# Kernel optimization log

Measured on AMD Instinct MI355X. Metric: run time of the kernel, lower is better.

The kernel has to match this reference:

```python
import jax, jax.numpy as jnp
import numpy as np

B, S, D = 2, 2048, 2048
NH = 16
HD = D // NH  # 128
MAX_POS = 4096
ROPE_THETA = 10000.0


def rotate_half(x):
    x1, x2 = x[..., : x.shape[-1] // 2], x[..., x.shape[-1] // 2 :]
    return jnp.concatenate((-x2, x1), axis=-1)


def rope_tables(dtype=jnp.float32):
    inv_freq = 1.0 / (ROPE_THETA ** (jnp.arange(0, HD, 2, dtype=jnp.float32) / HD))
    t = jnp.arange(MAX_POS, dtype=jnp.float32)
    freqs = jnp.outer(t, inv_freq)              # [MAX_POS, HD/2]
    emb = jnp.concatenate((freqs, freqs), axis=-1)  # [MAX_POS, HD]
    return jnp.cos(emb).astype(dtype), jnp.sin(emb).astype(dtype)


def setup_inputs() -> dict:
    key = jax.random.key(0)
    ks = jax.random.split(key, 9)
    sc = 0.02
    return {
        "hidden_states": jax.random.normal(ks[0], (B, S, D), jnp.float32),
        "position_ids": jnp.arange(B * S, dtype=jnp.int32).reshape(B, S),
        "Wq": jax.random.normal(ks[1], (D, D), jnp.float32) * sc,
        "bq": jax.random.normal(ks[2], (D,), jnp.float32) * sc,
        "Wk": jax.random.normal(ks[3], (D, D), jnp.float32) * sc,
        "bk": jax.random.normal(ks[4], (D,), jnp.float32) * sc,
        "Wv": jax.random.normal(ks[5], (D, D), jnp.float32) * sc,
        "bv": jax.random.normal(ks[6], (D,), jnp.float32) * sc,
        "Wo": jax.random.normal(ks[7], (D, D), jnp.float32) * sc,
    }


def reference(hidden_states, position_ids, Wq, bq, Wk, bk, Wv, bv, Wo):
    b, s, _ = hidden_states.shape
    # projections (torch Linear: x @ W.T + b)
    q = (hidden_states @ Wq.T + bq).reshape(b, s, NH, HD).transpose(0, 2, 1, 3)
    k = (hidden_states @ Wk.T + bk).reshape(b, s, NH, HD).transpose(0, 2, 1, 3)
    v = (hidden_states @ Wv.T + bv).reshape(b, s, NH, HD).transpose(0, 2, 1, 3)
    # RoPE
    cos_t, sin_t = rope_tables(hidden_states.dtype)
    cos = cos_t[position_ids][:, None, :, :]  # [B,1,S,HD]
    sin = sin_t[position_ids][:, None, :, :]
    q = q * cos + rotate_half(q) * sin
    k = k * cos + rotate_half(k) * sin
    # NOTE: faithful to the source bug — softmax is computed but its result is
    # discarded; the AV matmul uses the UNNORMALIZED scaled scores.
    attn_weights = jnp.einsum("bhqd,bhkd->bhqk", q, k) / (HD ** 0.5)
    _ = jax.nn.softmax(attn_weights.astype(jnp.float32), axis=-1)  # dead, as in source
    attn_output = jnp.einsum("bhqk,bhkd->bhqd", attn_weights, v)
    attn_output = attn_output.transpose(0, 2, 1, 3).reshape(b, s, D)
    return attn_output @ Wo.T
```

## Files before the change

kernel.cpp:

```cpp
#include <hip/hip_runtime.h>
#include <hip/hip_bf16.h>


typedef __attribute__((ext_vector_type(8))) short bf16x8s;
typedef __attribute__((ext_vector_type(4))) float f32x4;

__device__ __forceinline__ ushort f2bf(float f) {
    union { float f; unsigned int u; } x; x.f = f;
    unsigned int u = x.u;
    unsigned int r = (u + 0x7fffu + ((u >> 16) & 1u)) >> 16;
    return (ushort)r;
}
__device__ __forceinline__ float b2f(ushort u) {
    union { unsigned int u; float f; } x; x.u = ((unsigned int)u) << 16;
    return x.f;
}

__device__ __forceinline__ void gload_lds16(const void* g, void* l) {
    __builtin_amdgcn_global_load_lds((__attribute__((address_space(1))) const void*)g,
                                     (__attribute__((address_space(3))) void*)l, 16, 0, 0);
}

template<bool BIAS, bool OBF16>
__global__ __launch_bounds__(512, 2)
void gemm256(const ushort* __restrict__ A, const ushort* __restrict__ B,
             const float* __restrict__ bias, void* __restrict__ Cv,
             int K, int lda, int ldb, int ldc,
             long sAb, long sBb, long sCb)
{
    __shared__ char smem[131072];

    int z = blockIdx.z;
    const ushort* Ab = A + (size_t)sAb * z;
    const ushort* Bb = B + (size_t)sBb * z;
    size_t Coff = (size_t)sCb * z;

    int nwgx = gridDim.x;
    int nwg = nwgx * gridDim.y;
    int wg = blockIdx.y * nwgx + blockIdx.x;
    int swz = ((nwg & 7) == 0) ? (wg & 7) * (nwg >> 3) + (wg >> 3) : wg;
    int m0 = (swz % nwgx) * 256;
    int n0 = (swz / nwgx) * 256;

    int tid = threadIdx.x;
    int l = tid & 63, wid = tid >> 6;
    int wm = (wid >> 2) * 128;
    int wn = (wid & 3) * 64;
    int lr = l & 15, lj = l >> 4;

    int offA[8], offB[4];
#pragma unroll
    for (int m = 0; m < 8; m++) {
        int r = wm + m * 16 + lr;
        offA[m] = (r >> 1) * 128 + (((((r & 1) << 2) | lj) ^ ((r >> 1) & 7)) << 4);
    }
#pragma unroll
    for (int n = 0; n < 4; n++) {
        int r = wn + n * 16 + lr;
        offB[n] = (r >> 1) * 128 + (((((r & 1) << 2) | lj) ^ ((r >> 1) & 7)) << 4);
    }

    unsigned srcA0, srcA1, srcB0, srcB1;
    int dst0 = tid * 16, dst1 = dst0 + 8192;
    {
        int c0 = tid, c1 = tid + 512;
        int pr0 = c0 >> 3, up0 = (c0 & 7) ^ (pr0 & 7);
        int r0 = (pr0 << 1) | (up0 >> 2), j0 = up0 & 3;
        int pr1 = c1 >> 3, up1 = (c1 & 7) ^ (pr1 & 7);
        int r1 = (pr1 << 1) | (up1 >> 2), j1 = up1 & 3;
        srcA0 = (unsigned)(m0 + r0) * lda + j0 * 8;
        srcA1 = (unsigned)(m0 + r1) * lda + j1 * 8;
        srcB0 = (unsigned)(n0 + r0) * ldb + j0 * 8;
        srcB1 = (unsigned)(n0 + r1) * ldb + j1 * 8;
    }

    f32x4 acc[8][4];
#pragma unroll
    for (int m = 0; m < 8; m++)
#pragma unroll
        for (int n = 0; n < 4; n++)
            acc[m][n] = (f32x4){0.f, 0.f, 0.f, 0.f};

    int NT = K >> 6;

#define STAGE_A(ldsbyte, eoff) { \
    gload_lds16(Ab + srcA0 + (eoff), smem + (ldsbyte) + dst0); \
    gload_lds16(Ab + srcA1 + (eoff), smem + (ldsbyte) + dst1); }
#define STAGE_B(ldsbyte, eoff) { \
    gload_lds16(Bb + srcB0 + (eoff), smem + (ldsbyte) + dst0); \
    gload_lds16(Bb + srcB1 + (eoff), smem + (ldsbyte) + dst1); }
#define MFMA_HALF(mb) { \
    __builtin_amdgcn_s_setprio(1); \
    _Pragma("unroll") \
    for (int m = 0; m < 4; m++) \
        _Pragma("unroll") \
        for (int n = 0; n < 4; n++) \
            acc[(mb) + m][n] = __builtin_amdgcn_mfma_f32_16x16x32_bf16( \
                af[(mb) + m], bf[n], acc[(mb) + m][n], 0, 0, 0); \
    __builtin_amdgcn_s_setprio(0); }

    STAGE_A(0, 0);
    STAGE_B(32768, 0);
    STAGE_A(16384, 32);
    STAGE_B(49152, 32);
    asm volatile("s_waitcnt vmcnt(4)" ::: "memory");
    __builtin_amdgcn_s_barrier();

    for (int t = 0; t < NT; ++t) {
        int lb = (t & 1) << 16;
        int pb = lb ^ 65536;
        bool pf = (t + 1 < NT);
        unsigned eo = (unsigned)(t + 1) * 64;
        bf16x8s af[8], bf[4];

#pragma unroll
        for (int m = 0; m < 4; m++)
            af[m] = *(const bf16x8s*)(smem + lb + offA[m]);
#pragma unroll
        for (int n = 0; n < 4; n++)
            bf[n] = *(const bf16x8s*)(smem + lb + 32768 + offB[n]);
        if (pf) STAGE_A(pb, eo);
#pragma unroll
        for (int m = 4; m < 8; m++)
            af[m] = *(const bf16x8s*)(smem + lb + offA[m]);
        asm volatile("s_waitcnt lgkmcnt(4)" ::: "memory");
        __builtin_amdgcn_sched_barrier(0);
        MFMA_HALF(0);
        asm volatile("s_waitcnt lgkmcnt(0)" ::: "memory");
        __builtin_amdgcn_sched_barrier(0);
        MFMA_HALF(4);
        if (pf) STAGE_B(pb + 32768, eo);
        if (pf) asm volatile("s_waitcnt vmcnt(4)" ::: "memory");
        else    asm volatile("s_waitcnt vmcnt(0)" ::: "memory");
        __builtin_amdgcn_s_barrier();

#pragma unroll
        for (int m = 0; m < 4; m++)
            af[m] = *(const bf16x8s*)(smem + lb + 16384 + offA[m]);
#pragma unroll
        for (int n = 0; n < 4; n++)
            bf[n] = *(const bf16x8s*)(smem + lb + 49152 + offB[n]);
        if (pf) STAGE_A(pb + 16384, eo + 32);
#pragma unroll
        for (int m = 4; m < 8; m++)
            af[m] = *(const bf16x8s*)(smem + lb + 16384 + offA[m]);
        asm volatile("s_waitcnt lgkmcnt(4)" ::: "memory");
        __builtin_amdgcn_sched_barrier(0);
        MFMA_HALF(0);
        asm volatile("s_waitcnt lgkmcnt(0)" ::: "memory");
        __builtin_amdgcn_sched_barrier(0);
        MFMA_HALF(4);
        if (pf) {
            STAGE_B(pb + 49152, eo + 32);
            asm volatile("s_waitcnt vmcnt(4)" ::: "memory");
            __builtin_amdgcn_s_barrier();
        }
    }
#undef STAGE_A
#undef STAGE_B
#undef MFMA_HALF

    int rr = lj * 4;
#pragma unroll
    for (int m = 0; m < 8; m++) {
#pragma unroll
        for (int n = 0; n < 4; n++) {
            int gr = m0 + wm + m * 16 + rr;
            int gc = n0 + wn + n * 16 + lr;
            float bv = BIAS ? bias[gc] : 0.f;
#pragma unroll
            for (int r = 0; r < 4; r++) {
                float v = acc[m][n][r] + bv;
                size_t off = Coff + (size_t)(gr + r) * ldc + gc;
                if (OBF16) ((ushort*)Cv)[off] = f2bf(v);
                else       ((float*)Cv)[off]  = v;
            }
        }
    }
}

template<bool BIAS, bool OBF16, int BN>
__global__ __launch_bounds__(256)
void gemm_nt(const ushort* __restrict__ A, const ushort* __restrict__ B,
             const float* __restrict__ bias, void* __restrict__ Cv,
             int K, int lda, int ldb, int ldc, int ZH,
             long sAb, long sAh, long sBb, long sBh, long sCb, long sCh)
{
    __shared__ ushort As[128 * 32];
    __shared__ ushort Bs[BN * 32];

    int z  = blockIdx.z;
    int zb = z / ZH, zh = z - zb * ZH;
    const ushort* Ab = A + (size_t)(sAb * zb + sAh * zh);
    const ushort* Bb = B + (size_t)(sBb * zb + sBh * zh);
    size_t Coff = (size_t)(sCb * zb + sCh * zh);

    int m0 = blockIdx.x * 128, n0 = blockIdx.y * BN;
    int t = threadIdx.x;
    int l = t & 63, w = t >> 6;
    int wm, wn;
    if (BN == 128) { wm = (w >> 1) * 64; wn = (w & 1) * 64; }
    else           { wm = w * 32;        wn = 0; }
    constexpr int FM = (BN == 128) ? 4 : 2;
    constexpr int FN = 4;
    int lr = l & 15, lk = (l >> 4) * 8;

    f32x4 acc[FM][FN];
#pragma unroll
    for (int i = 0; i < FM; i++)
#pragma unroll
        for (int j = 0; j < FN; j++)
            acc[i][j] = (f32x4){0.f, 0.f, 0.f, 0.f};

    int c0 = t, c1 = t + 256;
    int r0 = c0 >> 2, k0c = (c0 & 3) * 8;
    int r1 = c1 >> 2, k1c = (c1 & 3) * 8;

    for (int kt = 0; kt < K; kt += 32) {
        __syncthreads();
        gload_lds16(Ab + (size_t)(m0 + r0) * lda + kt + k0c, &As[c0 * 8]);
        gload_lds16(Ab + (size_t)(m0 + r1) * lda + kt + k1c, &As[c1 * 8]);
        gload_lds16(Bb + (size_t)(n0 + r0) * ldb + kt + k0c, &Bs[c0 * 8]);
        if (BN == 128)
            gload_lds16(Bb + (size_t)(n0 + r1) * ldb + kt + k1c, &Bs[c1 * 8]);
        __syncthreads();

        bf16x8s af[FM], bf[FN];
#pragma unroll
        for (int i = 0; i < FM; i++)
            af[i] = *(const bf16x8s*)&As[(wm + i * 16 + lr) * 32 + lk];
#pragma unroll
        for (int i = 0; i < FN; i++)
            bf[i] = *(const bf16x8s*)&Bs[(wn + i * 16 + lr) * 32 + lk];
#pragma unroll
        for (int mi = 0; mi < FM; mi++)
#pragma unroll
            for (int ni = 0; ni < FN; ni++)
                acc[mi][ni] = __builtin_amdgcn_mfma_f32_16x16x32_bf16(
                    af[mi], bf[ni], acc[mi][ni], 0, 0, 0);
    }

    int rr = (l >> 4) * 4;
#pragma unroll
    for (int mi = 0; mi < FM; mi++) {
#pragma unroll
        for (int ni = 0; ni < FN; ni++) {
            int gr = m0 + wm + mi * 16 + rr;
            int gc = n0 + wn + ni * 16 + lr;
            float bv = BIAS ? bias[gc] : 0.f;
#pragma unroll
            for (int r = 0; r < 4; r++) {
                float v = acc[mi][ni][r] + bv;
                size_t off = Coff + (size_t)(gr + r) * ldc + gc;
                if (OBF16) ((ushort*)Cv)[off] = f2bf(v);
                else       ((float*)Cv)[off]  = v;
            }
        }
    }
}

__global__ __launch_bounds__(256)
void rope_qk(ushort* __restrict__ QKV, const int* __restrict__ pos,
             ushort* __restrict__ QB)
{
    int tid = blockIdx.x * 256 + threadIdx.x;
    int row = tid >> 7;
    int r = tid & 127;
    int h = r >> 3, j = r & 7;
    int d0 = j * 8;
    float p = (float)pos[row];
    size_t qb = (size_t)row * 6144 + h * 128 + d0;

    bf16x8s q1 = *(const bf16x8s*)&QKV[qb];
    bf16x8s q2 = *(const bf16x8s*)&QKV[qb + 64];
    bf16x8s k1 = *(const bf16x8s*)&QKV[qb + 2048];
    bf16x8s k2 = *(const bf16x8s*)&QKV[qb + 2048 + 64];
    bf16x8s oq1, oq2, ok1, ok2;
#pragma unroll
    for (int i = 0; i < 8; i++) {
        float d = (float)(d0 + i);
        float ang = p * exp2f(d * (-13.287712379549449f / 64.0f));
        float s, c;
        sincosf(ang, &s, &c);
        float a = b2f((ushort)q1[i]), b = b2f((ushort)q2[i]);
        oq1[i] = (short)f2bf(a * c - b * s);
        oq2[i] = (short)f2bf(b * c + a * s);
        float e = b2f((ushort)k1[i]), f = b2f((ushort)k2[i]);
        ok1[i] = (short)f2bf(e * c - f * s);
        ok2[i] = (short)f2bf(f * c + e * s);
    }
    size_t ob = (size_t)row * 2048 + h * 128 + d0;
    *(bf16x8s*)&QB[ob]      = oq1;
    *(bf16x8s*)&QB[ob + 64] = oq2;
    *(bf16x8s*)&QKV[qb + 2048]      = ok1;
    *(bf16x8s*)&QKV[qb + 2048 + 64] = ok2;
}

__global__ __launch_bounds__(256)
void ktv_partial(const ushort* __restrict__ QKV, float* __restrict__ part)
{
    int bh = blockIdx.x;
    int b = bh >> 4, h = bh & 15;
    int s0 = blockIdx.y * 128;
    const ushort* Kp = QKV + (size_t)(b * 2048 + s0) * 6144 + 2048 + h * 128;
    const ushort* Vp = Kp + 2048;

    __shared__ ushort Ks[32][128];
    __shared__ ushort Vs[32][128];

    int t = threadIdx.x;
    int tx = t & 15, ty = t >> 4;
    float acc[8][8];
#pragma unroll
    for (int i = 0; i < 8; i++)
#pragma unroll
        for (int j = 0; j < 8; j++) acc[i][j] = 0.f;

    for (int sb = 0; sb < 128; sb += 32) {
        __syncthreads();
#pragma unroll
        for (int i = 0; i < 2; i++) {
            int idx = t + i * 256;
            int rw = idx >> 4, c8 = (idx & 15) * 8;
            *(bf16x8s*)&Ks[rw][c8] = *(const bf16x8s*)&Kp[(size_t)(sb + rw) * 6144 + c8];
            *(bf16x8s*)&Vs[rw][c8] = *(const bf16x8s*)&Vp[(size_t)(sb + rw) * 6144 + c8];
        }
        __syncthreads();
        for (int ss = 0; ss < 32; ss++) {
            bf16x8s kvv = *(const bf16x8s*)&Ks[ss][tx * 8];
            bf16x8s vvv = *(const bf16x8s*)&Vs[ss][ty * 8];
            float kv[8], vv[8];
#pragma unroll
            for (int i = 0; i < 8; i++) { kv[i] = b2f((ushort)kvv[i]); vv[i] = b2f((ushort)vvv[i]); }
#pragma unroll
            for (int i = 0; i < 8; i++)
#pragma unroll
                for (int j = 0; j < 8; j++)
                    acc[i][j] += kv[i] * vv[j];
        }
    }
    float* pp = part + ((size_t)blockIdx.y * 32 + bh) * 16384;
#pragma unroll
    for (int i = 0; i < 8; i++)
#pragma unroll
        for (int j = 0; j < 8; j++)
            pp[(tx * 8 + i) * 128 + (ty * 8 + j)] = acc[i][j];
}

__global__ __launch_bounds__(256)
void reduce_ktv(const float* __restrict__ part, ushort* __restrict__ Mb)
{
    int i = blockIdx.x * 256 + threadIdx.x;
    float s = 0.f;
#pragma unroll
    for (int p = 0; p < 16; p++) s += part[(size_t)p * 524288 + i];
    Mb[i] = f2bf(s * 0.08838834764831845f);
}

__global__ __launch_bounds__(256)
void conv_f32_bf16(const float* __restrict__ in, ushort* __restrict__ out, int n4)
{
    int i = blockIdx.x * 256 + threadIdx.x;
    if (i >= n4) return;
    float4 v = ((const float4*)in)[i];
    ushort4 o;
    o.x = f2bf(v.x); o.y = f2bf(v.y); o.z = f2bf(v.z); o.w = f2bf(v.w);
    ((ushort4*)out)[i] = o;
}

__global__ __launch_bounds__(256)
void conv_weights(const float* __restrict__ w0, const float* __restrict__ w1,
                  const float* __restrict__ w2, const float* __restrict__ w3,
                  ushort* __restrict__ qkv, ushort* __restrict__ wo)
{
    int i = blockIdx.x * 256 + threadIdx.x;
    int id = i >> 20;
    int off = i & 1048575;
    const float* src = (id == 0) ? w0 : (id == 1) ? w1 : (id == 2) ? w2 : w3;
    float4 v = ((const float4*)src)[off];
    ushort4 o;
    o.x = f2bf(v.x); o.y = f2bf(v.y); o.z = f2bf(v.z); o.w = f2bf(v.w);
    if (id < 3) ((ushort4*)qkv)[(size_t)id * 1048576 + off] = o;
    else        ((ushort4*)wo)[off] = o;
}

__global__ __launch_bounds__(256)
void pack_bias(const float* __restrict__ bq, const float* __restrict__ bk,
               const float* __restrict__ bv, float* __restrict__ bqkv)
{
    int i = blockIdx.x * 256 + threadIdx.x;
    float v = (i < 2048) ? bq[i] : (i < 4096) ? bk[i - 2048] : bv[i - 4096];
    bqkv[i] = v;
}

extern "C" void kernel_launch(void* const* d_in, const int* in_sizes, int n_in,
                              void* d_out, int out_size, void* d_ws, size_t ws_size,
                              hipStream_t stream)
{
    const float* hs = (const float*)d_in[0];
    const int*  pos = (const int*)d_in[1];
    const float* Wq = (const float*)d_in[2];
    const float* bq = (const float*)d_in[3];
    const float* Wk = (const float*)d_in[4];
    const float* bk = (const float*)d_in[5];
    const float* Wv = (const float*)d_in[6];
    const float* bv = (const float*)d_in[7];
    const float* Wo = (const float*)d_in[8];
    float* out = (float*)d_out;
    char* ws = (char*)d_ws;

    ushort* HSB  = (ushort*)(ws + 0);
    ushort* QB   = (ushort*)(ws + 0);
    ushort* WQKV = (ushort*)(ws + 16777216);
    ushort* NT   = (ushort*)(ws + 16777216);
    ushort* WOB  = (ushort*)(ws + 41943040);
    float*  BQKV = (float*)(ws + 50331648);
    ushort* QKVB = (ushort*)(ws + 50356224);
    ushort* MB   = (ushort*)(ws + 100687872);
    float*  PART = out;

    dim3 blk(256);

    conv_f32_bf16<<<8192, blk, 0, stream>>>(hs, HSB, 2097152);
    conv_weights<<<16384, blk, 0, stream>>>(Wq, Wk, Wv, Wo, WQKV, WOB);
    pack_bias<<<24, blk, 0, stream>>>(bq, bk, bv, BQKV);

    gemm256<true, true><<<dim3(16, 24, 1), dim3(512), 0, stream>>>(
        HSB, WQKV, BQKV, QKVB, 2048, 2048, 2048, 6144, 0, 0, 0);

    rope_qk<<<2048, blk, 0, stream>>>(QKVB, pos, QB);

    ktv_partial<<<dim3(32, 16, 1), blk, 0, stream>>>(QKVB, PART);
    reduce_ktv<<<2048, blk, 0, stream>>>(PART, MB);

    gemm_nt<false, true, 128><<<dim3(16, 1, 32), blk, 0, stream>>>(
        WOB, MB, nullptr, NT, 128, 2048, 128, 2048, 16,
        0, 128, 262144, 16384, 4194304, 128);

    gemm256<false, false><<<dim3(8, 8, 2), dim3(512), 0, stream>>>(
        QB, NT, nullptr, out, 2048, 2048, 2048, 2048,
        4194304, 4194304, 4194304);
}
```

Before: 382.1 us.

## Shrink gemm256 K-stage to 32, precompute RoPE table, use gemm_nt for output GEMM

The main GEMM drops from a 64-wide K step in two half-stages to a single 32-wide double-buffered stage using 64KB of LDS. Its launch bound rises to 4 blocks per CU, aiming for higher occupancy. RoPE cos/sin values now come from a precomputed table built by a new kernel instead of per-element sincos/exp2. The final output GEMM switches from gemm256 to the 128-tile gemm_nt kernel. The single-stage loop waits on vmcnt(0) every iteration, which weakens load/compute overlap, and the 4-block bound may cause register spills with a 128-float accumulator per thread.

New measurement: 1.473 ms. 3.85x slower.

```diff
diff --git a/kernel.cpp b/kernel.cpp
--- a/kernel.cpp
+++ b/kernel.cpp
@@ -22,13 +22,13 @@
 }
 
 template<bool BIAS, bool OBF16>
-__global__ __launch_bounds__(512, 2)
+__global__ __launch_bounds__(512, 4)
 void gemm256(const ushort* __restrict__ A, const ushort* __restrict__ B,
              const float* __restrict__ bias, void* __restrict__ Cv,
              int K, int lda, int ldb, int ldc,
              long sAb, long sBb, long sCb)
 {
-    __shared__ char smem[131072];
+    __shared__ char smem[65536];
 
     int z = blockIdx.z;
     const ushort* Ab = A + (size_t)sAb * z;
@@ -81,7 +81,7 @@
         for (int n = 0; n < 4; n++)
             acc[m][n] = (f32x4){0.f, 0.f, 0.f, 0.f};
 
-    int NT = K >> 6;
+    int NT = K >> 5;
 
 #define STAGE_A(ldsbyte, eoff) { \
     gload_lds16(Ab + srcA0 + (eoff), smem + (ldsbyte) + dst0); \
@@ -100,61 +100,36 @@
     __builtin_amdgcn_s_setprio(0); }
 
     STAGE_A(0, 0);
-    STAGE_B(32768, 0);
-    STAGE_A(16384, 32);
-    STAGE_B(49152, 32);
-    asm volatile("s_waitcnt vmcnt(4)" ::: "memory");
+    STAGE_B(16384, 0);
+    asm volatile("s_waitcnt vmcnt(0)" ::: "memory");
     __builtin_amdgcn_s_barrier();
 
     for (int t = 0; t < NT; ++t) {
-        int lb = (t & 1) << 16;
-        int pb = lb ^ 65536;
+        int lb = (t & 1) << 15;
+        int pb = lb ^ 32768;
         bool pf = (t + 1 < NT);
-        unsigned eo = (unsigned)(t + 1) * 64;
+        unsigned eo = (unsigned)(t + 1) * 32;
         bf16x8s af[8], bf[4];
 
+#pragma unroll
+        for (int n = 0; n < 4; n++)
+            bf[n] = *(const bf16x8s*)(smem + lb + 16384 + offB[n]);
 #pragma unroll
         for (int m = 0; m < 4; m++)
             af[m] = *(const bf16x8s*)(smem + lb + offA[m]);
-#pragma unroll
-        for (int n = 0; n < 4; n++)
-            bf[n] = *(const bf16x8s*)(smem + lb + 32768 + offB[n]);
         if (pf) STAGE_A(pb, eo);
 #pragma unroll
         for (int m = 4; m < 8; m++)
             af[m] = *(const bf16x8s*)(smem + lb + offA[m]);
+        if (pf) STAGE_B(pb + 16384, eo);
         asm volatile("s_waitcnt lgkmcnt(4)" ::: "memory");
         __builtin_amdgcn_sched_barrier(0);
         MFMA_HALF(0);
         asm volatile("s_waitcnt lgkmcnt(0)" ::: "memory");
         __builtin_amdgcn_sched_barrier(0);
         MFMA_HALF(4);
-        if (pf) STAGE_B(pb + 32768, eo);
-        if (pf) asm volatile("s_waitcnt vmcnt(4)" ::: "memory");
-        else    asm volatile("s_waitcnt vmcnt(0)" ::: "memory");
+        asm volatile("s_waitcnt vmcnt(0)" ::: "memory");
         __builtin_amdgcn_s_barrier();
-
-#pragma unroll
-        for (int m = 0; m < 4; m++)
-            af[m] = *(const bf16x8s*)(smem + lb + 16384 + offA[m]);
-#pragma unroll
-        for (int n = 0; n < 4; n++)
-            bf[n] = *(const bf16x8s*)(smem + lb + 49152 + offB[n]);
-        if (pf) STAGE_A(pb + 16384, eo + 32);
-#pragma unroll
-        for (int m = 4; m < 8; m++)
-            af[m] = *(const bf16x8s*)(smem + lb + 16384 + offA[m]);
-        asm volatile("s_waitcnt lgkmcnt(4)" ::: "memory");
-        __builtin_amdgcn_sched_barrier(0);
-        MFMA_HALF(0);
-        asm volatile("s_waitcnt lgkmcnt(0)" ::: "memory");
-        __builtin_amdgcn_sched_barrier(0);
-        MFMA_HALF(4);
-        if (pf) {
-            STAGE_B(pb + 49152, eo + 32);
-            asm volatile("s_waitcnt vmcnt(4)" ::: "memory");
-            __builtin_amdgcn_s_barrier();
-        }
     }
 #undef STAGE_A
 #undef STAGE_B
@@ -260,15 +235,27 @@
 }
 
 __global__ __launch_bounds__(256)
+void build_rope_tab(float2* __restrict__ tab)
+{
+    int i = blockIdx.x * 256 + threadIdx.x;
+    int p = i >> 6, d = i & 63;
+    float ang = (float)p * exp2f((float)d * (-13.287712379549449f / 64.0f));
+    float s, c;
+    sincosf(ang, &s, &c);
+    tab[i] = make_float2(c, s);
+}
+
+__global__ __launch_bounds__(256)
 void rope_qk(ushort* __restrict__ QKV, const int* __restrict__ pos,
-             ushort* __restrict__ QB)
+             const float2* __restrict__ tab, ushort* __restrict__ QB)
 {
     int tid = blockIdx.x * 256 + threadIdx.x;
     int row = tid >> 7;
     int r = tid & 127;
     int h = r >> 3, j = r & 7;
     int d0 = j * 8;
-    float p = (float)pos[row];
+    int p = pos[row];
+    const float2* tp = tab + ((size_t)p << 6) + d0;
     size_t qb = (size_t)row * 6144 + h * 128 + d0;
 
     bf16x8s q1 = *(const bf16x8s*)&QKV[qb];
@@ -278,10 +265,8 @@
     bf16x8s oq1, oq2, ok1, ok2;
 #pragma unroll
     for (int i = 0; i < 8; i++) {
-        float d = (float)(d0 + i);
-        float ang = p * exp2f(d * (-13.287712379549449f / 64.0f));
-        float s, c;
-        sincosf(ang, &s, &c);
+        float2 cs = tp[i];
+        float c = cs.x, s = cs.y;
         float a = b2f((ushort)q1[i]), b = b2f((ushort)q2[i]);
         oq1[i] = (short)f2bf(a * c - b * s);
         oq2[i] = (short)f2bf(b * c + a * s);
@@ -417,10 +402,12 @@
     float*  BQKV = (float*)(ws + 50331648);
     ushort* QKVB = (ushort*)(ws + 50356224);
     ushort* MB   = (ushort*)(ws + 100687872);
+    float2* TAB  = (float2*)(ws + 101736448);
     float*  PART = out;
 
     dim3 blk(256);
 
+    build_rope_tab<<<1024, blk, 0, stream>>>(TAB);
     conv_f32_bf16<<<8192, blk, 0, stream>>>(hs, HSB, 2097152);
     conv_weights<<<16384, blk, 0, stream>>>(Wq, Wk, Wv, Wo, WQKV, WOB);
     pack_bias<<<24, blk, 0, stream>>>(bq, bk, bv, BQKV);
@@ -428,7 +415,7 @@
     gemm256<true, true><<<dim3(16, 24, 1), dim3(512), 0, stream>>>(
         HSB, WQKV, BQKV, QKVB, 2048, 2048, 2048, 6144, 0, 0, 0);
 
-    rope_qk<<<2048, blk, 0, stream>>>(QKVB, pos, QB);
+    rope_qk<<<2048, blk, 0, stream>>>(QKVB, pos, TAB, QB);
 
     ktv_partial<<<dim3(32, 16, 1), blk, 0, stream>>>(QKVB, PART);
     reduce_ktv<<<2048, blk, 0, stream>>>(PART, MB);
@@ -437,7 +424,7 @@
         WOB, MB, nullptr, NT, 128, 2048, 128, 2048, 16,
         0, 128, 262144, 16384, 4194304, 128);
 
-    gemm256<false, false><<<dim3(8, 8, 2), dim3(512), 0, stream>>>(
-        QB, NT, nullptr, out, 2048, 2048, 2048, 2048,
-        4194304, 4194304, 4194304);
-}
+    gemm_nt<false, false, 128><<<dim3(16, 16, 2), blk, 0, stream>>>(
+        QB, NT, nullptr, out, 2048, 2048, 2048, 2048, 1,
+        4194304, 0, 4194304, 0, 4194304, 0);
+}
```
